# Kernel optimization log

Measured on AMD Instinct MI355X. Metric: run time of the kernel, lower is better.

Reference implementation:

```python
import jax, jax.numpy as jnp
import numpy as np

DIM = 1024
HEAD_DIM = 64
NUM_HEADS = DIM // HEAD_DIM
SCALE = HEAD_DIM ** -0.5


def setup_inputs() -> dict:
    key = jax.random.key(0)
    ks = jax.random.split(key, 12)
    b, n = 4, 2048
    std = DIM ** -0.5
    inp = {
        'words': jax.random.normal(ks[0], (b, n, DIM), jnp.float32),
        'position': jax.random.normal(ks[1], (b, n, DIM), jnp.float32),
        'conscious': jax.random.normal(ks[2], (b, n, DIM), jnp.float32),
        # projection weights stored as [in, out] (torch Linear W^T)
        'w_wq': jax.random.normal(ks[3], (DIM, DIM), jnp.float32) * std,
        'w_wk': jax.random.normal(ks[4], (DIM, DIM), jnp.float32) * std,
        'w_wv': jax.random.normal(ks[5], (DIM, DIM), jnp.float32) * std,
        'w_pq': jax.random.normal(ks[6], (DIM, DIM), jnp.float32) * std,
        'w_pk': jax.random.normal(ks[7], (DIM, DIM), jnp.float32) * std,
        'w_cq': jax.random.normal(ks[8], (DIM, DIM), jnp.float32) * std,
        'w_ck': jax.random.normal(ks[9], (DIM, DIM), jnp.float32) * std,
        'w_out': jax.random.normal(ks[10], (DIM, DIM), jnp.float32) * std,
        'b_out': jax.random.normal(ks[11], (DIM,), jnp.float32) * 0.01,
    }
    return inp


def _heads(x):
    b, n, _ = x.shape
    return x.reshape(b, n, NUM_HEADS, HEAD_DIM).transpose(0, 2, 1, 3)  # b h n d


def reference(words, position, conscious, w_wq, w_wk, w_wv, w_pq, w_pk, w_cq, w_ck, w_out, b_out):
    # fused multi-source q/k: sum of three projections per source
    q = _heads(words @ w_wq + position @ w_pq + conscious @ w_cq)
    k = _heads(words @ w_wk + position @ w_pk + conscious @ w_ck)
    v = _heads(words @ w_wv)
    sim = jnp.einsum('bhid,bhjd->bhij', q, k) * SCALE
    attn = jax.nn.softmax(sim, axis=-1)
    out = jnp.einsum('bhij,bhjd->bhid', attn, v)
    b, h, n, d = out.shape
    out = out.transpose(0, 2, 1, 3).reshape(b, n, h * d)
    return out @ w_out + b_out
```

## Files before the change

kernel.cpp:

```cpp
#include <hip/hip_runtime.h>
#include <hip/hip_bf16.h>

typedef __bf16 bf16_t;
typedef __attribute__((ext_vector_type(8))) __bf16 bf16x8;
typedef __attribute__((ext_vector_type(4))) float f32x4;
typedef __attribute__((ext_vector_type(16))) float f32x16;

__device__ __forceinline__ void gld_lds16(const void* g, void* l) {
  __builtin_amdgcn_global_load_lds((const __attribute__((address_space(1))) void*)g,
                                   (__attribute__((address_space(3))) void*)l, 16, 0, 0);
}

__global__ __launch_bounds__(256) void cast_concat(
    const float* __restrict__ w, const float* __restrict__ p,
    const float* __restrict__ c, bf16_t* __restrict__ X)
{
  unsigned idx = blockIdx.x * 256u + threadIdx.x;
  unsigned src = idx >> 21;
  unsigned rem = idx & ((1u << 21) - 1);
  unsigned row = rem >> 8;
  unsigned k4  = (rem & 255u) * 4u;
  const float* s = (src == 0) ? w : (src == 1) ? p : c;
  f32x4 v = *(const f32x4*)(s + (size_t)row * 1024 + k4);
  ushort4 u;
  u.x = __builtin_bit_cast(unsigned short, (bf16_t)v[0]);
  u.y = __builtin_bit_cast(unsigned short, (bf16_t)v[1]);
  u.z = __builtin_bit_cast(unsigned short, (bf16_t)v[2]);
  u.w = __builtin_bit_cast(unsigned short, (bf16_t)v[3]);
  *(ushort4*)(X + (size_t)row * 3072 + src * 1024 + k4) = u;
}

__global__ __launch_bounds__(256) void transpose_all(
    const float* __restrict__ w_wq, const float* __restrict__ w_pq,
    const float* __restrict__ w_cq, const float* __restrict__ w_wk,
    const float* __restrict__ w_pk, const float* __restrict__ w_ck,
    const float* __restrict__ w_wv, const float* __restrict__ w_out,
    bf16_t* __restrict__ Wqkt, bf16_t* __restrict__ Wvt, bf16_t* __restrict__ Wot)
{
  __shared__ float t[32][33];
  const int z = blockIdx.z;
  const float* src; bf16_t* dst; int dstride, koff, roff;
  switch (z) {
    case 0: src = w_wq;  dst = Wqkt; dstride = 3072; koff = 0;    roff = 0;    break;
    case 1: src = w_pq;  dst = Wqkt; dstride = 3072; koff = 1024; roff = 0;    break;
    case 2: src = w_cq;  dst = Wqkt; dstride = 3072; koff = 2048; roff = 0;    break;
    case 3: src = w_wk;  dst = Wqkt; dstride = 3072; koff = 0;    roff = 1024; break;
    case 4: src = w_pk;  dst = Wqkt; dstride = 3072; koff = 1024; roff = 1024; break;
    case 5: src = w_ck;  dst = Wqkt; dstride = 3072; koff = 2048; roff = 1024; break;
    case 6: src = w_wv;  dst = Wvt;  dstride = 1024; koff = 0;    roff = 0;    break;
    default: src = w_out; dst = Wot; dstride = 1024; koff = 0;    roff = 0;    break;
  }
  int bx = blockIdx.x, by = blockIdx.y;
  int x = bx * 32 + threadIdx.x;
  int y0 = by * 32;
  for (int i = threadIdx.y; i < 32; i += 8)
    t[i][threadIdx.x] = src[(size_t)(y0 + i) * 1024 + x];
  __syncthreads();
  int n0 = bx * 32;
  for (int i = threadIdx.y; i < 32; i += 8)
    dst[(size_t)(n0 + i + roff) * dstride + koff + y0 + threadIdx.x] =
        (bf16_t)t[threadIdx.x][i];
}

__global__ __launch_bounds__(512, 2) void gemm256_qk(
    const bf16_t* __restrict__ A, int lda,
    const bf16_t* __restrict__ Bt, int K,
    bf16_t* __restrict__ Qo, bf16_t* __restrict__ Ko, float scale, int nbx)
{
  __shared__ bf16_t As[2][256 * 64];
  __shared__ bf16_t Bs[2][256 * 64];

  const int tid = threadIdx.x;
  const int wave = tid >> 6, lane = tid & 63;
  const int wm = wave >> 2, wn = wave & 3;
  const int lrow = lane & 15, lch = lane >> 4;

  const int nwg = gridDim.x, cpx = nwg >> 3;
  const int id  = blockIdx.x;
  const int swz = (id & 7) * cpx + (id >> 3);
  const int mb = swz / nbx, nb = swz % nbx;
  const int m0 = mb * 256, n0 = nb * 256;

  const int srow = tid >> 3, spp = tid & 7;

  auto STAGE = [&](int buf, int k0) {
#pragma unroll
    for (int i = 0; i < 4; ++i) {
      int r = i * 64 + srow;
      int gsw = (spp ^ (r & 7)) * 8;
      gld_lds16(A + (size_t)(m0 + r) * lda + k0 + gsw, &As[buf][r * 64 + spp * 8]);
    }
#pragma unroll
    for (int i = 0; i < 4; ++i) {
      int r = i * 64 + srow;
      int gsw = (spp ^ (r & 7)) * 8;
      gld_lds16(Bt + (size_t)(n0 + r) * K + k0 + gsw, &Bs[buf][r * 64 + spp * 8]);
    }
  };

  const int NT = K >> 6;
  STAGE(0, 0);
  STAGE(1, 64);

  f32x4 acc[8][4] = {};

  for (int kt = 0; kt < NT; ++kt) {
    const int cur = kt & 1;
    if (kt < NT - 1) {
      asm volatile("s_waitcnt vmcnt(8)" ::: "memory");
    } else {
      asm volatile("s_waitcnt vmcnt(0)" ::: "memory");
    }
    asm volatile("s_barrier" ::: "memory");

#pragma unroll
    for (int ks = 0; ks < 2; ++ks) {
      bf16x8 af[8], bfr[4];
#pragma unroll
      for (int m = 0; m < 8; ++m) {
        int r = wm * 128 + m * 16 + lrow;
        af[m] = *(const bf16x8*)&As[cur][r * 64 + (((ks * 4 + lch) ^ (r & 7)) * 8)];
      }
#pragma unroll
      for (int n = 0; n < 4; ++n) {
        int r = wn * 64 + n * 16 + lrow;
        bfr[n] = *(const bf16x8*)&Bs[cur][r * 64 + (((ks * 4 + lch) ^ (r & 7)) * 8)];
      }
      __builtin_amdgcn_s_setprio(1);
#pragma unroll
      for (int m = 0; m < 8; ++m)
#pragma unroll
        for (int n = 0; n < 4; ++n)
          acc[m][n] = __builtin_amdgcn_mfma_f32_16x16x32_bf16(af[m], bfr[n], acc[m][n], 0, 0, 0);
      __builtin_amdgcn_s_setprio(0);
    }

    asm volatile("s_waitcnt lgkmcnt(0)" ::: "memory");
    asm volatile("s_barrier" ::: "memory");
    if (kt + 2 < NT) STAGE(cur, (kt + 2) * 64);
  }

  const int g = lane >> 4, cl = lane & 15;
#pragma unroll
  for (int m = 0; m < 8; ++m) {
    int m_base = m0 + wm * 128 + m * 16 + g * 4;
    int bb = m_base >> 11, nn = m_base & 2047;
#pragma unroll
    for (int n = 0; n < 4; ++n) {
      int col = n0 + wn * 64 + n * 16 + cl;
      bf16_t* dst = (col < 1024) ? Qo : Ko;
      int cc2 = col & 1023;
      float sc = (col < 1024) ? scale : 1.0f;
      int h = cc2 >> 6, d = cc2 & 63;
      size_t base = ((size_t)(bb * 16 + h) * 2048 + nn) * 64 + d;
#pragma unroll
      for (int r = 0; r < 4; ++r)
        dst[base + (size_t)r * 64] = (bf16_t)(acc[m][n][r] * sc);
    }
  }
}

template<int EPI>
__global__ __launch_bounds__(512, 2) void gemm128x256(
    const bf16_t* __restrict__ A, int lda,
    const bf16_t* __restrict__ Bt, int K,
    void* __restrict__ Cout, const float* __restrict__ bias)
{
  __shared__ bf16_t As[2][128 * 64];
  __shared__ bf16_t Bs[2][256 * 64];

  const int tid = threadIdx.x;
  const int wave = tid >> 6, lane = tid & 63;
  const int wm = wave >> 2, wn = wave & 3;
  const int lrow = lane & 15, lch = lane >> 4;

  const int nwg = gridDim.x, cpx = nwg >> 3;
  const int id  = blockIdx.x;
  const int swz = (id & 7) * cpx + (id >> 3);
  const int mb = swz >> 2, nb = swz & 3;
  const int m0 = mb * 128, n0 = nb * 256;

  const int srow = tid >> 3, spp = tid & 7;

  auto STAGE = [&](int buf, int k0) {
#pragma unroll
    for (int i = 0; i < 2; ++i) {
      int r = i * 64 + srow;
      int gsw = (spp ^ (r & 7)) * 8;
      gld_lds16(A + (size_t)(m0 + r) * lda + k0 + gsw, &As[buf][r * 64 + spp * 8]);
    }
#pragma unroll
    for (int i = 0; i < 4; ++i) {
      int r = i * 64 + srow;
      int gsw = (spp ^ (r & 7)) * 8;
      gld_lds16(Bt + (size_t)(n0 + r) * K + k0 + gsw, &Bs[buf][r * 64 + spp * 8]);
    }
  };

  const int NT = K >> 6;
  STAGE(0, 0);
  STAGE(1, 64);

  f32x4 acc[4][4] = {};

  for (int kt = 0; kt < NT; ++kt) {
    const int cur = kt & 1;
    if (kt < NT - 1) {
      asm volatile("s_waitcnt vmcnt(6)" ::: "memory");
    } else {
      asm volatile("s_waitcnt vmcnt(0)" ::: "memory");
    }
    asm volatile("s_barrier" ::: "memory");

#pragma unroll
    for (int ks = 0; ks < 2; ++ks) {
      bf16x8 af[4], bfr[4];
#pragma unroll
      for (int m = 0; m < 4; ++m) {
        int r = wm * 64 + m * 16 + lrow;
        af[m] = *(const bf16x8*)&As[cur][r * 64 + (((ks * 4 + lch) ^ (r & 7)) * 8)];
      }
#pragma unroll
      for (int n = 0; n < 4; ++n) {
        int r = wn * 64 + n * 16 + lrow;
        bfr[n] = *(const bf16x8*)&Bs[cur][r * 64 + (((ks * 4 + lch) ^ (r & 7)) * 8)];
      }
      __builtin_amdgcn_s_setprio(1);
#pragma unroll
      for (int m = 0; m < 4; ++m)
#pragma unroll
        for (int n = 0; n < 4; ++n)
          acc[m][n] = __builtin_amdgcn_mfma_f32_16x16x32_bf16(af[m], bfr[n], acc[m][n], 0, 0, 0);
      __builtin_amdgcn_s_setprio(0);
    }

    asm volatile("s_waitcnt lgkmcnt(0)" ::: "memory");
    asm volatile("s_barrier" ::: "memory");
    if (kt + 2 < NT) STAGE(cur, (kt + 2) * 64);
  }

  const int g = lane >> 4, cl = lane & 15;
  if (EPI == 1) {
    bf16_t* Vo = (bf16_t*)Cout;
#pragma unroll
    for (int m = 0; m < 4; ++m) {
      int m_base = m0 + wm * 64 + m * 16 + g * 4;
      int bb = m_base >> 11, nn = m_base & 2047;
#pragma unroll
      for (int n = 0; n < 4; ++n) {
        int col = n0 + wn * 64 + n * 16 + cl;
        int h = col >> 6, d = col & 63;
        ushort4 u;
        u.x = __builtin_bit_cast(unsigned short, (bf16_t)acc[m][n][0]);
        u.y = __builtin_bit_cast(unsigned short, (bf16_t)acc[m][n][1]);
        u.z = __builtin_bit_cast(unsigned short, (bf16_t)acc[m][n][2]);
        u.w = __builtin_bit_cast(unsigned short, (bf16_t)acc[m][n][3]);
        *(ushort4*)(Vo + ((size_t)(bb * 16 + h) * 64 + d) * 2048 + nn) = u;
      }
    }
  } else {
    float* Co = (float*)Cout;
#pragma unroll
    for (int m = 0; m < 4; ++m) {
      int m_base = m0 + wm * 64 + m * 16 + g * 4;
#pragma unroll
      for (int n = 0; n < 4; ++n) {
        int col = n0 + wn * 64 + n * 16 + cl;
        float bv = bias[col];
#pragma unroll
        for (int r = 0; r < 4; ++r)
          Co[(size_t)(m_base + r) * 1024 + col] = acc[m][n][r] + bv;
      }
    }
  }
}

__global__ __launch_bounds__(256, 2) void attn_kernel(
    const bf16_t* __restrict__ Q, const bf16_t* __restrict__ Kb,
    const bf16_t* __restrict__ Vt, bf16_t* __restrict__ O)
{
  __shared__ bf16_t Ks[2][64 * 64];
  __shared__ bf16_t Vs[2][64 * 64];

  const int fid = blockIdx.x;
  const int swz = (fid & 7) * 64 + (fid >> 3);
  const int bh = swz >> 3, qt = swz & 7;
  const int bb = bh >> 4, h = bh & 15;

  const int tid = threadIdx.x, wave = tid >> 6, lane = tid & 63;
  const int lq = lane & 31;
  const int lh = lane >> 5;

  const bf16_t* Qb    = Q  + ((size_t)bh * 2048 + qt * 256) * 64;
  const bf16_t* Kbase = Kb + (size_t)bh * 2048 * 64;
  const bf16_t* Vbase = Vt + (size_t)bh * 64 * 2048;

  const int srow = tid >> 3, spp = tid & 7;

  auto STAGE_K = [&](int buf, int tile) {
#pragma unroll
    for (int i = 0; i < 2; ++i) {
      int r = i * 32 + srow;
      int sg = (spp ^ (r & 7)) * 8;
      gld_lds16(Kbase + (size_t)(tile * 64 + r) * 64 + sg, &Ks[buf][i * 2048 + tid * 8]);
    }
  };
  auto STAGE_V = [&](int buf, int tile) {
#pragma unroll
    for (int i = 0; i < 2; ++i) {
      int r = i * 32 + srow;
      int sg = (spp ^ (r & 7)) * 8;
      gld_lds16(Vbase + (size_t)r * 2048 + tile * 64 + sg, &Vs[buf][i * 2048 + tid * 8]);
    }
  };

  STAGE_K(0, 0); STAGE_V(0, 0); STAGE_K(1, 1);

  bf16x8 qf0[4], qf1[4];
#pragma unroll
  for (int kf = 0; kf < 4; ++kf) {
    qf0[kf] = *(const bf16x8*)(Qb + (size_t)(wave * 64 + lq) * 64 + kf * 16 + lh * 8);
    qf1[kf] = *(const bf16x8*)(Qb + (size_t)(wave * 64 + 32 + lq) * 64 + kf * 16 + lh * 8);
  }

  f32x16 acc0[2] = {}, acc1[2] = {};
  float m0r = -1.0e30f, l0r = 0.f, m1r = -1.0e30f, l1r = 0.f;
  bf16x8 pb0[4], pb1[4];

  auto QKT2 = [&](int tile, f32x16 (&s0)[2], f32x16 (&s1)[2]) {
    const int kb = tile & 1;
#pragma unroll
    for (int nb2 = 0; nb2 < 2; ++nb2) {
      int r = nb2 * 32 + lq;
      f32x16 z0 = {}, z1 = {};
#pragma unroll
      for (int kf = 0; kf < 4; ++kf) {
        bf16x8 ka = *(const bf16x8*)&Ks[kb][r * 64 + (((kf * 2 + lh) ^ (r & 7)) * 8)];
        z0 = __builtin_amdgcn_mfma_f32_32x32x16_bf16(ka, qf0[kf], z0, 0, 0, 0);
        z1 = __builtin_amdgcn_mfma_f32_32x32x16_bf16(ka, qf1[kf], z1, 0, 0, 0);
      }
      s0[nb2] = z0; s1[nb2] = z1;
    }
  };

  auto PV2 = [&](int tile) {
    const int vb = tile & 1;
#pragma unroll
    for (int ks = 0; ks < 4; ++ks)
#pragma unroll
      for (int db = 0; db < 2; ++db) {
        int r = db * 32 + lq;
        bf16x8 va = *(const bf16x8*)&Vs[vb][r * 64 + (((ks * 2 + lh) ^ (r & 7)) * 8)];
        acc0[db] = __builtin_amdgcn_mfma_f32_32x32x16_bf16(va, pb0[ks], acc0[db], 0, 0, 0);
        acc1[db] = __builtin_amdgcn_mfma_f32_32x32x16_bf16(va, pb1[ks], acc1[db], 0, 0, 0);
      }
  };

  auto SOFTMAX = [&](f32x16 (&st)[2], float& mr, float& lr,
                     f32x16 (&ac)[2], bf16x8 (&po)[4]) {
    float tmax = fmaxf(st[0][0], st[0][1]);
#pragma unroll
    for (int nb2 = 0; nb2 < 2; ++nb2)
#pragma unroll
      for (int rg = (nb2 ? 0 : 2); rg < 16; rg += 2)
        tmax = fmaxf(fmaxf(tmax, st[nb2][rg]), st[nb2][rg + 1]);
    tmax = fmaxf(tmax, __shfl_xor(tmax, 32));

    if (!__all(tmax <= mr + 8.0f)) {
      float mnew = fmaxf(mr, tmax);
      float corr = __builtin_amdgcn_exp2f(mr - mnew);
      mr = mnew;
      lr *= corr;
#pragma unroll
      for (int db = 0; db < 2; ++db)
#pragma unroll
        for (int rg = 0; rg < 16; ++rg)
          ac[db][rg] *= corr;
    }

    float sm = 0.f;
#pragma unroll
    for (int nb2 = 0; nb2 < 2; ++nb2)
#pragma unroll
      for (int rg = 0; rg < 16; ++rg) {
        float p = __builtin_amdgcn_exp2f(st[nb2][rg] - mr);
        st[nb2][rg] = p;
        sm += p;
      }
    sm += __shfl_xor(sm, 32);
    lr += sm;

#pragma unroll
    for (int ks = 0; ks < 4; ++ks) {
      const int nb2 = ks >> 1;
      const int R = (ks & 1) * 8;
      unsigned x0, x1, y0, y1;
      asm("v_cvt_pk_bf16_f32 %0, %1, %2" : "=v"(x0) : "v"(st[nb2][R + 0]), "v"(st[nb2][R + 1]));
      asm("v_cvt_pk_bf16_f32 %0, %1, %2" : "=v"(x1) : "v"(st[nb2][R + 2]), "v"(st[nb2][R + 3]));
      asm("v_cvt_pk_bf16_f32 %0, %1, %2" : "=v"(y0) : "v"(st[nb2][R + 4]), "v"(st[nb2][R + 5]));
      asm("v_cvt_pk_bf16_f32 %0, %1, %2" : "=v"(y1) : "v"(st[nb2][R + 6]), "v"(st[nb2][R + 7]));
      asm volatile("v_permlane32_swap_b32 %0, %1" : "+v"(x0), "+v"(y0));
      asm volatile("v_permlane32_swap_b32 %0, %1" : "+v"(x1), "+v"(y1));
      int4 pw;
      pw.x = (int)x0; pw.y = (int)x1; pw.z = (int)y0; pw.w = (int)y1;
      po[ks] = __builtin_bit_cast(bf16x8, pw);
    }
  };

  asm volatile("s_waitcnt vmcnt(0)" ::: "memory");
  __builtin_amdgcn_s_barrier();
  asm volatile("" ::: "memory");
  {
    f32x16 s0[2], s1[2];
    QKT2(0, s0, s1);
    SOFTMAX(s0, m0r, l0r, acc0, pb0);
    SOFTMAX(s1, m1r, l1r, acc1, pb1);
  }
  asm volatile("s_waitcnt lgkmcnt(0)" ::: "memory");
  __builtin_amdgcn_s_barrier();
  asm volatile("" ::: "memory");

  for (int t = 0; t < 32; ++t) {
    if (t < 30)       { STAGE_V((t + 1) & 1, t + 1); STAGE_K(t & 1, t + 2); }
    else if (t == 30) { STAGE_V(1, 31); }
    if (t < 30)       asm volatile("s_waitcnt vmcnt(4)" ::: "memory");
    else if (t == 30) asm volatile("s_waitcnt vmcnt(2)" ::: "memory");
    else              asm volatile("s_waitcnt vmcnt(0)" ::: "memory");
    __builtin_amdgcn_s_barrier();
    asm volatile("" ::: "memory");

    f32x16 s0[2], s1[2];
    __builtin_amdgcn_s_setprio(1);
    if (t < 31) QKT2(t + 1, s0, s1);
    PV2(t);
    __builtin_amdgcn_s_setprio(0);
    if (t < 31) {
      SOFTMAX(s0, m0r, l0r, acc0, pb0);
      SOFTMAX(s1, m1r, l1r, acc1, pb1);
    }

    asm volatile("s_waitcnt lgkmcnt(0)" ::: "memory");
    __builtin_amdgcn_s_barrier();
    asm volatile("" ::: "memory");
  }

  float inv0 = 1.0f / l0r, inv1 = 1.0f / l1r;
#pragma unroll
  for (int qb = 0; qb < 2; ++qb) {
    float inv = qb ? inv1 : inv0;
    int nn = qt * 256 + wave * 64 + qb * 32 + lq;
    size_t obase = ((size_t)bb * 2048 + nn) * 1024 + h * 64;
#pragma unroll
    for (int db = 0; db < 2; ++db)
#pragma unroll
      for (int rr = 0; rr < 4; ++rr) {
        f32x16& a = qb ? acc1[db] : acc0[db];
        ushort4 u;
        u.x = __builtin_bit_cast(unsigned short, (bf16_t)(a[rr * 4 + 0] * inv));
        u.y = __builtin_bit_cast(unsigned short, (bf16_t)(a[rr * 4 + 1] * inv));
        u.z = __builtin_bit_cast(unsigned short, (bf16_t)(a[rr * 4 + 2] * inv));
        u.w = __builtin_bit_cast(unsigned short, (bf16_t)(a[rr * 4 + 3] * inv));
        *(ushort4*)(O + obase + db * 32 + rr * 8 + lh * 4) = u;
      }
  }
}

extern "C" void kernel_launch(void* const* d_in, const int* in_sizes, int n_in,
                              void* d_out, int out_size, void* d_ws, size_t ws_size,
                              hipStream_t stream) {
  const float* words     = (const float*)d_in[0];
  const float* position  = (const float*)d_in[1];
  const float* conscious = (const float*)d_in[2];
  const float* w_wq  = (const float*)d_in[3];
  const float* w_wk  = (const float*)d_in[4];
  const float* w_wv  = (const float*)d_in[5];
  const float* w_pq  = (const float*)d_in[6];
  const float* w_pk  = (const float*)d_in[7];
  const float* w_cq  = (const float*)d_in[8];
  const float* w_ck  = (const float*)d_in[9];
  const float* w_out = (const float*)d_in[10];
  const float* b_out = (const float*)d_in[11];

  char* ws = (char*)d_ws;
  bf16_t* Xcat = (bf16_t*)(ws);
  bf16_t* Wqkt = (bf16_t*)(ws + 50331648);
  bf16_t* Wvt  = (bf16_t*)(ws + 62914560);
  bf16_t* Wot  = (bf16_t*)(ws + 65011712);
  bf16_t* Qb   = (bf16_t*)(ws + 67108864);
  bf16_t* Kbf  = (bf16_t*)(ws + 83886080);
  bf16_t* Vtb  = (bf16_t*)(ws + 100663296);
  bf16_t* Ob   = (bf16_t*)(ws + 117440512);

  cast_concat<<<24576, 256, 0, stream>>>(words, position, conscious, Xcat);

  transpose_all<<<dim3(32, 32, 8), dim3(32, 8), 0, stream>>>(
      w_wq, w_pq, w_cq, w_wk, w_pk, w_ck, w_wv, w_out, Wqkt, Wvt, Wot);

  gemm256_qk<<<256, 512, 0, stream>>>(Xcat, 3072, Wqkt, 3072, Qb, Kbf,
                                      0.125f * 1.44269504f, 8);
  gemm128x256<1><<<256, 512, 0, stream>>>(Xcat, 3072, Wvt, 1024, Vtb, nullptr);

  attn_kernel<<<512, 256, 0, stream>>>(Qb, Kbf, Vtb, Ob);

  gemm128x256<2><<<256, 512, 0, stream>>>(Ob, 1024, Wot, 1024, (float*)d_out, b_out);
}
```

Measured before the change: 281.7 us.

## Interleave A/B tile prefetch with MFMA phases in projection GEMM main loop

The GEMM K-loop is split into four phases, each computing two 16-row M sub-tiles. Global-to-LDS loads are spread across those phases: the next A tile is loaded one step ahead into the other buffer, and the B tile is loaded two steps ahead into the current buffer once its fragments are already in registers. The aim is to overlap memory traffic with MFMA work instead of issuing one large staging burst at the end of each iteration. The cost is more barriers per K-step (two per phase) and a more intricate vmcnt wait scheme.

```diff
diff --git a/kernel.cpp b/kernel.cpp
--- a/kernel.cpp
+++ b/kernel.cpp
@@ -83,61 +83,76 @@
 
   const int srow = tid >> 3, spp = tid & 7;
 
-  auto STAGE = [&](int buf, int k0) {
-#pragma unroll
-    for (int i = 0; i < 4; ++i) {
-      int r = i * 64 + srow;
+  auto STAGE_A = [&](int buf, int k0, int h) {
+#pragma unroll
+    for (int i = 0; i < 2; ++i) {
+      int r = h * 128 + i * 64 + srow;
       int gsw = (spp ^ (r & 7)) * 8;
       gld_lds16(A + (size_t)(m0 + r) * lda + k0 + gsw, &As[buf][r * 64 + spp * 8]);
     }
-#pragma unroll
-    for (int i = 0; i < 4; ++i) {
-      int r = i * 64 + srow;
+  };
+  auto STAGE_B = [&](int buf, int k0, int h) {
+#pragma unroll
+    for (int i = 0; i < 2; ++i) {
+      int r = h * 128 + i * 64 + srow;
       int gsw = (spp ^ (r & 7)) * 8;
       gld_lds16(Bt + (size_t)(n0 + r) * K + k0 + gsw, &Bs[buf][r * 64 + spp * 8]);
     }
   };
 
   const int NT = K >> 6;
-  STAGE(0, 0);
-  STAGE(1, 64);
+  STAGE_A(0, 0, 0); STAGE_A(0, 0, 1);
+  STAGE_B(0, 0, 0); STAGE_B(0, 0, 1);
+  STAGE_B(1, 64, 0); STAGE_B(1, 64, 1);
+  asm volatile("s_waitcnt vmcnt(4)" ::: "memory");
+  asm volatile("s_barrier" ::: "memory");
 
   f32x4 acc[8][4] = {};
 
   for (int kt = 0; kt < NT; ++kt) {
-    const int cur = kt & 1;
-    if (kt < NT - 1) {
-      asm volatile("s_waitcnt vmcnt(8)" ::: "memory");
-    } else {
-      asm volatile("s_waitcnt vmcnt(0)" ::: "memory");
-    }
-    asm volatile("s_barrier" ::: "memory");
-
-#pragma unroll
-    for (int ks = 0; ks < 2; ++ks) {
-      bf16x8 af[8], bfr[4];
-#pragma unroll
-      for (int m = 0; m < 8; ++m) {
-        int r = wm * 128 + m * 16 + lrow;
-        af[m] = *(const bf16x8*)&As[cur][r * 64 + (((ks * 4 + lch) ^ (r & 7)) * 8)];
-      }
-#pragma unroll
-      for (int n = 0; n < 4; ++n) {
-        int r = wn * 64 + n * 16 + lrow;
-        bfr[n] = *(const bf16x8*)&Bs[cur][r * 64 + (((ks * 4 + lch) ^ (r & 7)) * 8)];
-      }
+    const int cur = kt & 1, nxt = cur ^ 1;
+    bf16x8 bfr[4][2];
+
+#pragma unroll
+    for (int p = 0; p < 4; ++p) {
+      bf16x8 af[2][2];
+#pragma unroll
+      for (int j = 0; j < 2; ++j)
+#pragma unroll
+        for (int ks = 0; ks < 2; ++ks) {
+          int r = wm * 128 + (p * 2 + j) * 16 + lrow;
+          af[j][ks] = *(const bf16x8*)&As[cur][r * 64 + (((ks * 4 + lch) ^ (r & 7)) * 8)];
+        }
+      if (p == 0) {
+#pragma unroll
+        for (int n = 0; n < 4; ++n)
+#pragma unroll
+          for (int ks = 0; ks < 2; ++ks) {
+            int r = wn * 64 + n * 16 + lrow;
+            bfr[n][ks] = *(const bf16x8*)&Bs[cur][r * 64 + (((ks * 4 + lch) ^ (r & 7)) * 8)];
+          }
+      }
+      if (p == 0 && kt + 1 < NT) STAGE_A(nxt, (kt + 1) * 64, 0);
+      if (p == 1 && kt + 1 < NT) STAGE_A(nxt, (kt + 1) * 64, 1);
+      if (p == 2 && kt + 2 < NT) STAGE_B(cur, (kt + 2) * 64, 0);
+      if (p == 3 && kt + 2 < NT) STAGE_B(cur, (kt + 2) * 64, 1);
+      if (p == 3) {
+        if (kt + 2 < NT)      asm volatile("s_waitcnt vmcnt(4)" ::: "memory");
+        else                  asm volatile("s_waitcnt vmcnt(0)" ::: "memory");
+      }
+      asm volatile("s_barrier" ::: "memory");
       __builtin_amdgcn_s_setprio(1);
 #pragma unroll
-      for (int m = 0; m < 8; ++m)
-#pragma unroll
-        for (int n = 0; n < 4; ++n)
-          acc[m][n] = __builtin_amdgcn_mfma_f32_16x16x32_bf16(af[m], bfr[n], acc[m][n], 0, 0, 0);
+      for (int ks = 0; ks < 2; ++ks)
+#pragma unroll
+        for (int j = 0; j < 2; ++j)
+#pragma unroll
+          for (int n = 0; n < 4; ++n)
+            acc[p * 2 + j][n] = __builtin_amdgcn_mfma_f32_16x16x32_bf16(
+                af[j][ks], bfr[n][ks], acc[p * 2 + j][n], 0, 0, 0);
       __builtin_amdgcn_s_setprio(0);
-    }
-
-    asm volatile("s_waitcnt lgkmcnt(0)" ::: "memory");
-    asm volatile("s_barrier" ::: "memory");
-    if (kt + 2 < NT) STAGE(cur, (kt + 2) * 64);
+      asm volatile("s_barrier" ::: "memory");
+    }
   }
 
   const int g = lane >> 4, cl = lane & 15;
```

Measured after the change: 276.7 us. About the same (-1.8%).
